# Performance work log

Measured on AMD Instinct MI355X. Metric: run time of the kernel, lower is better.

The kernel has to match this reference:

```python
import jax, jax.numpy as jnp
import numpy as np

VOCAB, HID, LSTM_H, T_LEN, N_LAB, BATCH = 21128, 768, 128, 256, 9, 32


def _gru_dir(x, Wih, Whh, bih, bhh):
    # x: [B,T,D]; PyTorch GRU gate order: reset, update, new
    xp = jnp.einsum('btd,gd->tbg', x, Wih) + bih  # [T,B,3H]
    H = Whh.shape[1]
    def step(h, xt):
        gh = h @ Whh.T + bhh
        xr, xz, xn = jnp.split(xt, 3, axis=-1)
        hr, hz, hn = jnp.split(gh, 3, axis=-1)
        r = jax.nn.sigmoid(xr + hr)
        z = jax.nn.sigmoid(xz + hz)
        n = jnp.tanh(xn + r * hn)
        hnew = (1.0 - z) * n + z * h
        return hnew, hnew
    h0 = jnp.zeros((x.shape[0], H), x.dtype)
    _, hs = jax.lax.scan(step, h0, xp)
    return hs  # [T,B,H]


def _crf_llh(emissions, labels, trans, start, end):
    # emissions [B,T,L], labels [B,T]; full mask (all ones)
    e = jnp.transpose(emissions, (1, 0, 2))  # [T,B,L]
    emit_scores = jnp.take_along_axis(e, labels.T[:, :, None], axis=2)[:, :, 0]  # [T,B]
    trans_scores = trans[labels[:, :-1], labels[:, 1:]]  # [B,T-1]
    num = start[labels[:, 0]] + emit_scores.sum(0) + trans_scores.sum(1) + end[labels[:, -1]]
    def step(alpha, et):
        alpha = jax.nn.logsumexp(alpha[:, :, None] + trans[None] + et[:, None, :], axis=1)
        return alpha, None
    alpha0 = start + e[0]
    alpha, _ = jax.lax.scan(step, alpha0, e[1:])
    denom = jax.nn.logsumexp(alpha + end, axis=1)
    return num - denom  # [B]


def _viterbi(emissions, trans, start, end):
    e = jnp.transpose(emissions, (1, 0, 2))  # [T,B,L]
    def step(alpha, et):
        scores = alpha[:, :, None] + trans[None]  # [B,L_prev,L_cur]
        bp = jnp.argmax(scores, axis=1)
        alpha = jnp.max(scores, axis=1) + et
        return alpha, bp
    alpha0 = start + e[0]
    alpha, bps = jax.lax.scan(step, alpha0, e[1:])  # bps: [T-1,B,L]
    last = jnp.argmax(alpha + end, axis=1)  # [B]
    def back(y, bp):
        yprev = jnp.take_along_axis(bp, y[:, None], axis=1)[:, 0]
        return yprev, yprev
    _, path = jax.lax.scan(back, last, bps, reverse=True)  # [T-1,B]
    return jnp.concatenate([path, last[None]], axis=0).T  # [B,T]


def setup_inputs() -> dict:
    key = jax.random.key(0)
    ks = jax.random.split(key, 16)
    s = 0.02
    inp = {
        'input_ids': jax.random.randint(ks[0], (BATCH, T_LEN), 0, VOCAB),
        'attention_mask': jnp.ones((BATCH, T_LEN), jnp.int64 if jax.config.jax_enable_x64 else jnp.int32),
        'labels': jax.random.randint(ks[1], (BATCH, T_LEN), 0, N_LAB),
        'emb': jax.random.normal(ks[2], (VOCAB, HID), jnp.float32) * s,
        'Wih_f': jax.random.normal(ks[3], (3 * LSTM_H, HID), jnp.float32) * s,
        'Whh_f': jax.random.normal(ks[4], (3 * LSTM_H, LSTM_H), jnp.float32) * s,
        'bih_f': jnp.zeros((3 * LSTM_H,), jnp.float32),
        'bhh_f': jnp.zeros((3 * LSTM_H,), jnp.float32),
        'Wih_b': jax.random.normal(ks[5], (3 * LSTM_H, HID), jnp.float32) * s,
        'Whh_b': jax.random.normal(ks[6], (3 * LSTM_H, LSTM_H), jnp.float32) * s,
        'bih_b': jnp.zeros((3 * LSTM_H,), jnp.float32),
        'bhh_b': jnp.zeros((3 * LSTM_H,), jnp.float32),
        'Wlin': jax.random.normal(ks[7], (N_LAB, 2 * LSTM_H), jnp.float32) * s,
        'blin': jnp.zeros((N_LAB,), jnp.float32),
        'trans': jax.random.normal(ks[8], (N_LAB, N_LAB), jnp.float32) * 0.1,
        'start': jax.random.normal(ks[9], (N_LAB,), jnp.float32) * 0.1,
        'end': jax.random.normal(ks[10], (N_LAB,), jnp.float32) * 0.1,
    }
    return inp


def reference(input_ids, attention_mask, labels, emb, Wih_f, Whh_f, bih_f, bhh_f,
              Wih_b, Whh_b, bih_b, bhh_b, Wlin, blin, trans, start, end):
    x = emb[input_ids]  # [B,T,HID]
    hf = _gru_dir(x, Wih_f, Whh_f, bih_f, bhh_f)                 # [T,B,H]
    hb = _gru_dir(x[:, ::-1, :], Wih_b, Whh_b, bih_b, bhh_b)[::-1]  # [T,B,H]
    seq = jnp.concatenate([hf, hb], axis=-1).transpose(1, 0, 2)  # [B,T,2H]
    emissions = seq @ Wlin.T + blin                              # [B,T,L]
    decoded = _viterbi(emissions, trans, start, end)             # [B,T] int
    llh = _crf_llh(emissions, labels, trans, start, end)         # [B]
    loss = -jnp.mean(llh)
    return decoded, loss
```

## Files before the change

### kernel.cpp

```cpp
#include <hip/hip_runtime.h>
#include <math.h>

#define T_LEN 256
#define BATCH 32
#define HID   768
#define GH    384
#define LH    128
#define NLAB  9
#define M_TOT (T_LEN*BATCH)

typedef float v2f __attribute__((ext_vector_type(2)));
typedef _Float16 h8 __attribute__((ext_vector_type(8)));
typedef float f4 __attribute__((ext_vector_type(4)));

#define LO_SCALE 1024.f
#define LO_INV   (1.f/1024.f)

#define BC(x, i) __int_as_float(__builtin_amdgcn_ds_swizzle(__float_as_int(x), (i) << 5))

#define BAR_LGKM() do {                                   \
    asm volatile("s_waitcnt lgkmcnt(0)" ::: "memory");    \
    __builtin_amdgcn_s_barrier();                         \
    asm volatile("" ::: "memory");                        \
  } while (0)

__global__ __launch_bounds__(256, 2) void k_gemm_xp(
    const int* __restrict__ ids, const float* __restrict__ emb,
    const float* __restrict__ Wf, const float* __restrict__ Wb,
    const float* __restrict__ bihf, const float* __restrict__ bihb,
    float* __restrict__ xp)
{
  __shared__ __align__(16) _Float16 Ah[128*40];
  __shared__ __align__(16) _Float16 Al[128*40];
  __shared__ __align__(16) _Float16 Bh[128*40];
  __shared__ __align__(16) _Float16 Bl[128*40];

  const int tid  = threadIdx.x;
  const int lane = tid & 63, w = tid >> 6;
  const int m0 = blockIdx.y * 128, n0 = blockIdx.x * 128;

  const int srow = tid >> 1, sk = (tid & 1) * 16;
  const int gm = m0 + srow;
  const int tok = ids[(gm & 31) * T_LEN + (gm >> 5)];
  const float* aG = emb + (size_t)tok * HID + sk;
  const int gn = n0 + srow;
  const float* bG = (gn < GH ? Wf + (size_t)gn * HID
                             : Wb + (size_t)(gn - GH) * HID) + sk;

  const int fr = lane & 15, fq = lane >> 4;
  const int mrow = (w & 1) * 64;
  const int ncol = (w >> 1) * 64;

  f4 acc[4][4];
  f4 acc2[4][4];
#pragma unroll
  for (int i = 0; i < 4; ++i)
#pragma unroll
    for (int j = 0; j < 4; ++j) { acc[i][j] = f4{0,0,0,0}; acc2[i][j] = f4{0,0,0,0}; }

  const int sb = srow * 40 + sk;

  float4 ra[4], rb[4];
#pragma unroll
  for (int c = 0; c < 4; ++c) {
    ra[c] = *reinterpret_cast<const float4*>(aG + 4 * c);
    rb[c] = *reinterpret_cast<const float4*>(bG + 4 * c);
  }

  for (int kt = 0; kt < HID / 32; ++kt) {
    BAR_LGKM();
#pragma unroll
    for (int m = 0; m < 2; ++m) {
      const float4* src = m ? rb : ra;
      _Float16* dsth = m ? Bh : Ah;
      _Float16* dstl = m ? Bl : Al;
#pragma unroll
      for (int seg = 0; seg < 2; ++seg) {
        float xs[8] = {src[2*seg].x, src[2*seg].y, src[2*seg].z, src[2*seg].w,
                       src[2*seg+1].x, src[2*seg+1].y, src[2*seg+1].z, src[2*seg+1].w};
        h8 hi, lo;
#pragma unroll
        for (int c = 0; c < 8; ++c) {
          _Float16 h = (_Float16)xs[c];
          hi[c] = h;
          lo[c] = (_Float16)((xs[c] - (float)h) * LO_SCALE);
        }
        *reinterpret_cast<h8*>(&dsth[sb + seg * 8]) = hi;
        *reinterpret_cast<h8*>(&dstl[sb + seg * 8]) = lo;
      }
    }
    if (kt + 1 < HID / 32) {
      const float* pa = aG + (kt + 1) * 32;
      const float* pb = bG + (kt + 1) * 32;
#pragma unroll
      for (int c = 0; c < 4; ++c) {
        ra[c] = *reinterpret_cast<const float4*>(pa + 4 * c);
        rb[c] = *reinterpret_cast<const float4*>(pb + 4 * c);
      }
    }
    BAR_LGKM();

    h8 fbh[4], fbl[4];
#pragma unroll
    for (int j = 0; j < 4; ++j) {
      const int off = (ncol + j * 16 + fr) * 40 + fq * 8;
      fbh[j] = *reinterpret_cast<const h8*>(&Bh[off]);
      fbl[j] = *reinterpret_cast<const h8*>(&Bl[off]);
    }
#pragma unroll
    for (int i = 0; i < 4; ++i) {
      const int off = (mrow + i * 16 + fr) * 40 + fq * 8;
      h8 fah = *reinterpret_cast<const h8*>(&Ah[off]);
      h8 fal = *reinterpret_cast<const h8*>(&Al[off]);
#pragma unroll
      for (int j = 0; j < 4; ++j) {
        acc[i][j]  = __builtin_amdgcn_mfma_f32_16x16x32_f16(fah, fbh[j], acc[i][j],  0, 0, 0);
        acc2[i][j] = __builtin_amdgcn_mfma_f32_16x16x32_f16(fah, fbl[j], acc2[i][j], 0, 0, 0);
        acc2[i][j] = __builtin_amdgcn_mfma_f32_16x16x32_f16(fal, fbh[j], acc2[i][j], 0, 0, 0);
      }
    }
  }

  float bcol[4];
#pragma unroll
  for (int j = 0; j < 4; ++j) {
    const int c = n0 + ncol + j * 16 + fr;
    bcol[j] = (c < GH) ? bihf[c] : bihb[c - GH];
  }
#pragma unroll
  for (int i = 0; i < 4; ++i)
#pragma unroll
    for (int j = 0; j < 4; ++j) {
      const int col = n0 + ncol + j * 16 + fr;
#pragma unroll
      for (int r = 0; r < 4; ++r) {
        const int row = m0 + mrow + i * 16 + fq * 4 + r;
        xp[(size_t)row * HID + col] = acc[i][j][r] + acc2[i][j][r] * LO_INV + bcol[j];
      }
    }
}

__global__ __attribute__((amdgpu_flat_work_group_size(512, 512),
                          amdgpu_waves_per_eu(2, 2)))
void k_gru(
    const float* __restrict__ xp,
    const float* __restrict__ Whhf, const float* __restrict__ Whhb,
    const float* __restrict__ bhhf, const float* __restrict__ bhhb,
    float* __restrict__ hbuf, float* __restrict__ lossp)
{
  __shared__ __align__(1024) float hsp[2][256];
  const int tid = threadIdx.x;
  const int g   = tid >> 2;
  const int q   = tid & 3;
  const int bd  = blockIdx.x;
  const int dir = bd >> 5, b = bd & 31;
  const float* Whh = dir ? Whhb : Whhf;
  const float* bhh = dir ? bhhb : bhhf;

  if (bd == 0 && tid == 0) *lossp = 0.f;

  const float br = bhh[g], bz = bhh[g + LH], bn = bhh[g + 2*LH];
  const float* wg0 = Whh + (size_t)(0*LH + g) * LH + q * 32;
  const float* wg1 = Whh + (size_t)(1*LH + g) * LH + q * 32;
  const float* wg2 = Whh + (size_t)(2*LH + g) * LH + q * 32;

  const int t0 = dir ? (T_LEN - 1) : 0;
  const int dt = dir ? -1 : 1;
  const float* px = xp + (size_t)t0 * BATCH * HID + b * HID + dir * GH + g;
  float*       ph = hbuf + (size_t)t0 * BATCH * 256 + b * 256 + dir * LH + g;

  const long long xs = (long long)dt * BATCH * HID * 4;
  const long long hs = (long long)dt * BATCH * 256 * 4;
  const unsigned xslo = (unsigned)(xs & 0xffffffffll);
  const int      xshi = (int)(xs >> 32);
  const unsigned hslo = (unsigned)(hs & 0xffffffffll);
  const int      hshi = (int)(hs >> 32);
  const unsigned xlo = (unsigned)(uintptr_t)px, xhi = (unsigned)((uintptr_t)px >> 32);
  const unsigned hlo = (unsigned)(uintptr_t)ph, hhi = (unsigned)((uintptr_t)ph >> 32);
  const unsigned rd0 = (unsigned)(uintptr_t)(&hsp[0][36 * q]);
  const unsigned wr0 = (unsigned)(uintptr_t)(&hsp[1][36 * (g >> 5) + (g & 31)]);

  if (tid < LH) hsp[0][36 * (tid >> 5) + (tid & 31)] = 0.f;
  BAR_LGKM();

  int cnt = T_LEN;
  asm volatile(
    "global_load_dwordx4 v[128:131], %[wg0], off\n\t"
    "global_load_dwordx4 v[132:135], %[wg0], off offset:16\n\t"
    "global_load_dwordx4 v[136:139], %[wg0], off offset:32\n\t"
    "global_load_dwordx4 v[140:143], %[wg0], off offset:48\n\t"
    "global_load_dwordx4 v[144:147], %[wg0], off offset:64\n\t"
    "global_load_dwordx4 v[148:151], %[wg0], off offset:80\n\t"
    "global_load_dwordx4 v[152:155], %[wg0], off offset:96\n\t"
    "global_load_dwordx4 v[156:159], %[wg0], off offset:112\n\t"
    "global_load_dwordx4 v[160:163], %[wg1], off\n\t"
    "global_load_dwordx4 v[164:167], %[wg1], off offset:16\n\t"
    "global_load_dwordx4 v[168:171], %[wg1], off offset:32\n\t"
    "global_load_dwordx4 v[172:175], %[wg1], off offset:48\n\t"
    "global_load_dwordx4 v[176:179], %[wg1], off offset:64\n\t"
    "global_load_dwordx4 v[180:183], %[wg1], off offset:80\n\t"
    "global_load_dwordx4 v[184:187], %[wg1], off offset:96\n\t"
    "global_load_dwordx4 v[188:191], %[wg1], off offset:112\n\t"
    "global_load_dwordx4 v[192:195], %[wg2], off\n\t"
    "global_load_dwordx4 v[196:199], %[wg2], off offset:16\n\t"
    "global_load_dwordx4 v[200:203], %[wg2], off offset:32\n\t"
    "global_load_dwordx4 v[204:207], %[wg2], off offset:48\n\t"
    "global_load_dwordx4 v[208:211], %[wg2], off offset:64\n\t"
    "global_load_dwordx4 v[212:215], %[wg2], off offset:80\n\t"
    "global_load_dwordx4 v[216:219], %[wg2], off offset:96\n\t"
    "global_load_dwordx4 v[220:223], %[wg2], off offset:112\n\t"
    "v_mov_b32 v96, %[xlo]\n\t"
    "v_mov_b32 v97, %[xhi]\n\t"
    "v_mov_b32 v98, %[hlo]\n\t"
    "v_mov_b32 v99, %[hhi]\n\t"
    "v_mov_b32 v100, %[rd0]\n\t"
    "v_mov_b32 v101, %[wr0]\n\t"
    "global_load_dword v107, v[96:97], off\n\t"
    "global_load_dword v108, v[96:97], off offset:512\n\t"
    "global_load_dword v109, v[96:97], off offset:1024\n\t"
    "v_mov_b32 v110, 0\n\t"
    "s_waitcnt vmcnt(0)\n\t"
    "0:\n\t"
    "s_waitcnt vmcnt(1)\n\t"
    "v_mov_b32 v104, v107\n\t"
    "v_mov_b32 v105, v108\n\t"
    "v_mov_b32 v106, v109\n\t"
    "ds_read_b128 v[224:227], v100\n\t"
    "ds_read_b128 v[228:231], v100 offset:16\n\t"
    "ds_read_b128 v[232:235], v100 offset:32\n\t"
    "ds_read_b128 v[236:239], v100 offset:48\n\t"
    "ds_read_b128 v[240:243], v100 offset:64\n\t"
    "ds_read_b128 v[244:247], v100 offset:80\n\t"
    "ds_read_b128 v[248:251], v100 offset:96\n\t"
    "ds_read_b128 v[252:255], v100 offset:112\n\t"
    "s_cmp_lg_u32 %[cnt], 1\n\t"
    "s_cbranch_scc0 2f\n\t"
    "v_add_co_u32 v96, vcc, %[xslo], v96\n\t"
    "v_addc_co_u32 v97, vcc, %[xshi], v97, vcc\n\t"
    "global_load_dword v107, v[96:97], off\n\t"
    "global_load_dword v108, v[96:97], off offset:512\n\t"
    "global_load_dword v109, v[96:97], off offset:1024\n\t"
    "2:\n\t"
    "s_waitcnt lgkmcnt(0)\n\t"
    "v_pk_mul_f32 v[116:117], v[128:129], v[224:225]\n\t"
    "v_pk_mul_f32 v[118:119], v[130:131], v[226:227]\n\t"
    "v_pk_fma_f32 v[116:117], v[132:133], v[228:229], v[116:117]\n\t"
    "v_pk_fma_f32 v[118:119], v[134:135], v[230:231], v[118:119]\n\t"
    "v_pk_fma_f32 v[116:117], v[136:137], v[232:233], v[116:117]\n\t"
    "v_pk_fma_f32 v[118:119], v[138:139], v[234:235], v[118:119]\n\t"
    "v_pk_fma_f32 v[116:117], v[140:141], v[236:237], v[116:117]\n\t"
    "v_pk_fma_f32 v[118:119], v[142:143], v[238:239], v[118:119]\n\t"
    "v_pk_fma_f32 v[116:117], v[144:145], v[240:241], v[116:117]\n\t"
    "v_pk_fma_f32 v[118:119], v[146:147], v[242:243], v[118:119]\n\t"
    "v_pk_fma_f32 v[116:117], v[148:149], v[244:245], v[116:117]\n\t"
    "v_pk_fma_f32 v[118:119], v[150:151], v[246:247], v[118:119]\n\t"
    "v_pk_fma_f32 v[116:117], v[152:153], v[248:249], v[116:117]\n\t"
    "v_pk_fma_f32 v[118:119], v[154:155], v[250:251], v[118:119]\n\t"
    "v_pk_fma_f32 v[116:117], v[156:157], v[252:253], v[116:117]\n\t"
    "v_pk_fma_f32 v[118:119], v[158:159], v[254:255], v[118:119]\n\t"
    "v_pk_mul_f32 v[120:121], v[160:161], v[224:225]\n\t"
    "v_pk_mul_f32 v[122:123], v[162:163], v[226:227]\n\t"
    "v_pk_fma_f32 v[120:121], v[164:165], v[228:229], v[120:121]\n\t"
    "v_pk_fma_f32 v[122:123], v[166:167], v[230:231], v[122:123]\n\t"
    "v_pk_fma_f32 v[120:121], v[168:169], v[232:233], v[120:121]\n\t"
    "v_pk_fma_f32 v[122:123], v[170:171], v[234:235], v[122:123]\n\t"
    "v_pk_fma_f32 v[120:121], v[172:173], v[236:237], v[120:121]\n\t"
    "v_pk_fma_f32 v[122:123], v[174:175], v[238:239], v[122:123]\n\t"
    "v_pk_fma_f32 v[120:121], v[176:177], v[240:241], v[120:121]\n\t"
    "v_pk_fma_f32 v[122:123], v[178:179], v[242:243], v[122:123]\n\t"
    "v_pk_fma_f32 v[120:121], v[180:181], v[244:245], v[120:121]\n\t"
    "v_pk_fma_f32 v[122:123], v[182:183], v[246:247], v[122:123]\n\t"
    "v_pk_fma_f32 v[120:121], v[184:185], v[248:249], v[120:121]\n\t"
    "v_pk_fma_f32 v[122:123], v[186:187], v[250:251], v[122:123]\n\t"
    "v_pk_fma_f32 v[120:121], v[188:189], v[252:253], v[120:121]\n\t"
    "v_pk_fma_f32 v[122:123], v[190:191], v[254:255], v[122:123]\n\t"
    "v_pk_mul_f32 v[124:125], v[192:193], v[224:225]\n\t"
    "v_pk_mul_f32 v[126:127], v[194:195], v[226:227]\n\t"
    "v_pk_fma_f32 v[124:125], v[196:197], v[228:229], v[124:125]\n\t"
    "v_pk_fma_f32 v[126:127], v[198:199], v[230:231], v[126:127]\n\t"
    "v_pk_fma_f32 v[124:125], v[200:201], v[232:233], v[124:125]\n\t"
    "v_pk_fma_f32 v[126:127], v[202:203], v[234:235], v[126:127]\n\t"
    "v_pk_fma_f32 v[124:125], v[204:205], v[236:237], v[124:125]\n\t"
    "v_pk_fma_f32 v[126:127], v[206:207], v[238:239], v[126:127]\n\t"
    "v_pk_fma_f32 v[124:125], v[208:209], v[240:241], v[124:125]\n\t"
    "v_pk_fma_f32 v[126:127], v[210:211], v[242:243], v[126:127]\n\t"
    "v_pk_fma_f32 v[124:125], v[212:213], v[244:245], v[124:125]\n\t"
    "v_pk_fma_f32 v[126:127], v[214:215], v[246:247], v[126:127]\n\t"
    "v_pk_fma_f32 v[124:125], v[216:217], v[248:249], v[124:125]\n\t"
    "v_pk_fma_f32 v[126:127], v[218:219], v[250:251], v[126:127]\n\t"
    "v_pk_fma_f32 v[124:125], v[220:221], v[252:253], v[124:125]\n\t"
    "v_pk_fma_f32 v[126:127], v[222:223], v[254:255], v[126:127]\n\t"
    "v_add_f32 v116, v116, v117\n\t"
    "v_add_f32 v118, v118, v119\n\t"
    "v_add_f32 v116, v116, v118\n\t"
    "v_add_f32 v120, v120, v121\n\t"
    "v_add_f32 v122, v122, v123\n\t"
    "v_add_f32 v120, v120, v122\n\t"
    "v_add_f32 v124, v124, v125\n\t"
    "v_add_f32 v126, v126, v127\n\t"
    "v_add_f32 v124, v124, v126\n\t"
    "ds_swizzle_b32 v111, v116 offset:0x041F\n\t"
    "ds_swizzle_b32 v112, v120 offset:0x041F\n\t"
    "ds_swizzle_b32 v113, v124 offset:0x041F\n\t"
    "s_waitcnt lgkmcnt(0)\n\t"
    "v_add_f32 v116, v116, v111\n\t"
    "v_add_f32 v120, v120, v112\n\t"
    "v_add_f32 v124, v124, v113\n\t"
    "ds_swizzle_b32 v111, v116 offset:0x081F\n\t"
    "ds_swizzle_b32 v112, v120 offset:0x081F\n\t"
    "ds_swizzle_b32 v113, v124 offset:0x081F\n\t"
    "s_waitcnt lgkmcnt(0)\n\t"
    "v_add_f32 v116, v116, v111\n\t"
    "v_add_f32 v120, v120, v112\n\t"
    "v_add_f32 v124, v124, v113\n\t"
    "v_add_f32 v111, v104, v116\n\t"
    "v_add_f32 v112, v105, v120\n\t"
    "v_add_f32 v113, v124, %[bn]\n\t"
    "v_add_f32 v111, v111, %[br]\n\t"
    "v_add_f32 v112, v112, %[bz]\n\t"
    "v_mul_f32 v111, 0xbfb8aa3b, v111\n\t"
    "v_mul_f32 v112, 0xbfb8aa3b, v112\n\t"
    "v_exp_f32 v111, v111\n\t"
    "v_exp_f32 v112, v112\n\t"
    "s_nop 0\n\t"
    "v_add_f32 v111, 1.0, v111\n\t"
    "v_add_f32 v112, 1.0, v112\n\t"
    "v_rcp_f32 v111, v111\n\t"
    "v_rcp_f32 v112, v112\n\t"
    "s_nop 0\n\t"
    "v_fmac_f32 v106, v111, v113\n\t"
    "v_mul_f32 v113, 0x4038aa3b, v106\n\t"
    "v_exp_f32 v113, v113\n\t"
    "v_sub_f32 v115, 1.0, v112\n\t"
    "s_nop 0\n\t"
    "v_add_f32 v114, -1.0, v113\n\t"
    "v_add_f32 v113, 1.0, v113\n\t"
    "v_rcp_f32 v113, v113\n\t"
    "s_nop 1\n\t"
    "v_mul_f32 v114, v114, v113\n\t"
    "v_mul_f32 v115, v115, v114\n\t"
    "v_fmac_f32 v115, v112, v110\n\t"
    "v_mov_b32 v110, v115\n\t"
    "ds_write_b32 v101, v115\n\t"
    "global_store_dword v[98:99], v115, off\n\t"
    "v_add_co_u32 v98, vcc, %[hslo], v98\n\t"
    "v_addc_co_u32 v99, vcc, %[hshi], v99, vcc\n\t"
    "v_xor_b32 v100, 0x400, v100\n\t"
    "v_xor_b32 v101, 0x400, v101\n\t"
    "s_waitcnt lgkmcnt(0)\n\t"
    "s_barrier\n\t"
    "s_sub_u32 %[cnt], %[cnt], 1\n\t"
    "s_cmp_lg_u32 %[cnt], 0\n\t"
    "s_cbranch_scc1 0b\n\t"
    : [cnt]"+s"(cnt)
    : [wg0]"v"(wg0), [wg1]"v"(wg1), [wg2]"v"(wg2),
      [xlo]"v"(xlo), [xhi]"v"(xhi), [hlo]"v"(hlo), [hhi]"v"(hhi),
      [rd0]"v"(rd0), [wr0]"v"(wr0),
      [br]"v"(br), [bz]"v"(bz), [bn]"v"(bn),
      [xslo]"s"(xslo), [xshi]"v"(xshi), [hslo]"s"(hslo), [hshi]"v"(hshi)
    : "memory", "vcc", "scc",
      "v96","v97","v98","v99","v100","v101","v102","v103","v104","v105",
      "v106","v107","v108","v109","v110","v111","v112","v113","v114","v115",
      "v116","v117","v118","v119","v120","v121","v122","v123","v124","v125",
      "v126","v127","v128","v129","v130","v131","v132","v133","v134","v135",
      "v136","v137","v138","v139","v140","v141","v142","v143","v144","v145",
      "v146","v147","v148","v149","v150","v151","v152","v153","v154","v155",
      "v156","v157","v158","v159","v160","v161","v162","v163","v164","v165",
      "v166","v167","v168","v169","v170","v171","v172","v173","v174","v175",
      "v176","v177","v178","v179","v180","v181","v182","v183","v184","v185",
      "v186","v187","v188","v189","v190","v191","v192","v193","v194","v195",
      "v196","v197","v198","v199","v200","v201","v202","v203","v204","v205",
      "v206","v207","v208","v209","v210","v211","v212","v213","v214","v215",
      "v216","v217","v218","v219","v220","v221","v222","v223","v224","v225",
      "v226","v227","v228","v229","v230","v231","v232","v233","v234","v235",
      "v236","v237","v238","v239","v240","v241","v242","v243","v244","v245",
      "v246","v247","v248","v249","v250","v251","v252","v253","v254","v255");
}

__global__ __launch_bounds__(256, 1) void k_crf_fused(
    const float* __restrict__ hbuf, const float* __restrict__ Wlin,
    const float* __restrict__ blin, const int* __restrict__ labels,
    const float* __restrict__ trans, const float* __restrict__ start,
    const float* __restrict__ endv, float* __restrict__ dec_out,
    float* __restrict__ lossp)
{
  __shared__ float el[T_LEN * 10];
  __shared__ __align__(16) unsigned char bp8[(T_LEN - 1) * 16];
  const int b    = blockIdx.x;
  const int tid  = threadIdx.x;
  const int lane = tid & 63, w = tid >> 6;
  const int sub  = lane >> 4, l16 = lane & 15;

  float4 wreg[NLAB][4];
#pragma unroll
  for (int j = 0; j < NLAB; ++j)
#pragma unroll
    for (int c = 0; c < 4; ++c)
      wreg[j][c] = *reinterpret_cast<const float4*>(Wlin + j * 256 + l16 * 16 + c * 4);

  for (int k = 0; k < 16; ++k) {
    const int t = w * 64 + k * 4 + sub;
    const float* hp = hbuf + ((size_t)t * BATCH + b) * 256 + l16 * 16;
    const float4 h0 = *reinterpret_cast<const float4*>(hp);
    const float4 h1 = *reinterpret_cast<const float4*>(hp + 4);
    const float4 h2 = *reinterpret_cast<const float4*>(hp + 8);
    const float4 h3 = *reinterpret_cast<const float4*>(hp + 12);
    float acc[NLAB];
#pragma unroll
    for (int j = 0; j < NLAB; ++j) {
      const float4 w0 = wreg[j][0], w1 = wreg[j][1], w2 = wreg[j][2], w3 = wreg[j][3];
      float s0 = h0.x*w0.x + h0.y*w0.y + h0.z*w0.z + h0.w*w0.w;
      float s1 = h1.x*w1.x + h1.y*w1.y + h1.z*w1.z + h1.w*w1.w;
      float s2 = h2.x*w2.x + h2.y*w2.y + h2.z*w2.z + h2.w*w2.w;
      float s3 = h3.x*w3.x + h3.y*w3.y + h3.z*w3.z + h3.w*w3.w;
      acc[j] = (s0 + s1) + (s2 + s3);
    }
#pragma unroll
    for (int j = 0; j < NLAB; ++j) {
#pragma unroll
      for (int off = 1; off < 16; off <<= 1)
        acc[j] += __shfl_xor(acc[j], off);
    }
    if (l16 < NLAB) {
      float v = acc[0];
#pragma unroll
      for (int j = 1; j < NLAB; ++j) v = (l16 == j) ? acc[j] : v;
      el[t * 10 + l16] = v + blin[l16];
    }
  }
  __syncthreads();

  if (w == 0) {
    float tcol[NLAB];
#pragma unroll
    for (int i = 0; i < NLAB; ++i)
      tcol[i] = (lane < NLAB) ? trans[i * NLAB + lane] : 0.f;
    float alpha = (lane < NLAB) ? (start[lane] + el[lane]) : -3e38f;
    float et_next = (lane < NLAB) ? el[10 + lane] : 0.f;
    for (int s = 0; s < T_LEN - 1; ++s) {
      const float et = et_next;
      if (s < T_LEN - 2)
        et_next = (lane < NLAB) ? el[(s + 2) * 10 + lane] : 0.f;
      float v[NLAB];
      v[0] = BC(alpha, 0) + tcol[0];
      v[1] = BC(alpha, 1) + tcol[1];
      v[2] = BC(alpha, 2) + tcol[2];
      v[3] = BC(alpha, 3) + tcol[3];
      v[4] = BC(alpha, 4) + tcol[4];
      v[5] = BC(alpha, 5) + tcol[5];
      v[6] = BC(alpha, 6) + tcol[6];
      v[7] = BC(alpha, 7) + tcol[7];
      v[8] = BC(alpha, 8) + tcol[8];
      float v01 = (v[0] >= v[1]) ? v[0] : v[1];  int i01 = (v[0] >= v[1]) ? 0 : 1;
      float v23 = (v[2] >= v[3]) ? v[2] : v[3];  int i23 = (v[2] >= v[3]) ? 2 : 3;
      float v45 = (v[4] >= v[5]) ? v[4] : v[5];  int i45 = (v[4] >= v[5]) ? 4 : 5;
      float v67 = (v[6] >= v[7]) ? v[6] : v[7];  int i67 = (v[6] >= v[7]) ? 6 : 7;
      float va = (v01 >= v23) ? v01 : v23;       int ia = (v01 >= v23) ? i01 : i23;
      float vb = (v45 >= v67) ? v45 : v67;       int ib = (v45 >= v67) ? i45 : i67;
      float vc = (va >= vb) ? va : vb;           int ic = (va >= vb) ? ia : ib;
      float best = (vc >= v[8]) ? vc : v[8];     int bi = (vc >= v[8]) ? ic : 8;
      alpha = best + et;
      if (lane < NLAB) bp8[s * 16 + lane] = (unsigned char)bi;
    }
    float fin = alpha + ((lane < NLAB) ? endv[lane] : 0.f);
    float fv[NLAB];
    fv[0] = BC(fin, 0); fv[1] = BC(fin, 1); fv[2] = BC(fin, 2);
    fv[3] = BC(fin, 3); fv[4] = BC(fin, 4); fv[5] = BC(fin, 5);
    fv[6] = BC(fin, 6); fv[7] = BC(fin, 7); fv[8] = BC(fin, 8);
    float f01 = (fv[0] >= fv[1]) ? fv[0] : fv[1];  int j01 = (fv[0] >= fv[1]) ? 0 : 1;
    float f23 = (fv[2] >= fv[3]) ? fv[2] : fv[3];  int j23 = (fv[2] >= fv[3]) ? 2 : 3;
    float f45 = (fv[4] >= fv[5]) ? fv[4] : fv[5];  int j45 = (fv[4] >= fv[5]) ? 4 : 5;
    float f67 = (fv[6] >= fv[7]) ? fv[6] : fv[7];  int j67 = (fv[6] >= fv[7]) ? 6 : 7;
    float fa = (f01 >= f23) ? f01 : f23;           int ja = (f01 >= f23) ? j01 : j23;
    float fb = (f45 >= f67) ? f45 : f67;           int jb = (f45 >= f67) ? j45 : j67;
    float fc = (fa >= fb) ? fa : fb;               int jc = (fa >= fb) ? ja : jb;
    int last = (fc >= fv[8]) ? jc : 8;
    if (lane == 0) {
      int y = last;
      dec_out[b * T_LEN + (T_LEN - 1)] = (float)y;
      uint4 row = *reinterpret_cast<const uint4*>(&bp8[(T_LEN - 2) * 16]);
      for (int s = T_LEN - 2; s >= 0; --s) {
        uint4 nrow = row;
        if (s > 0) nrow = *reinterpret_cast<const uint4*>(&bp8[(s - 1) * 16]);
        unsigned wsel = (y < 4) ? row.x : ((y < 8) ? row.y : row.z);
        y = (int)((wsel >> ((y & 3) * 8)) & 0xffu);
        dec_out[b * T_LEN + s] = (float)y;
        row = nrow;
      }
    }
  } else if (w == 1) {
    float tcol[NLAB];
#pragma unroll
    for (int i = 0; i < NLAB; ++i)
      tcol[i] = (lane < NLAB) ? trans[i * NLAB + lane] : 0.f;
    float ca = (lane < NLAB) ? (start[lane] + el[lane]) : -3e38f;
    float et_next = (lane < NLAB) ? el[10 + lane] : 0.f;
    for (int s = 0; s < T_LEN - 1; ++s) {
      const float et = et_next;
      if (s < T_LEN - 2)
        et_next = (lane < NLAB) ? el[(s + 2) * 10 + lane] : 0.f;
      float c[NLAB];
      c[0] = BC(ca, 0) + tcol[0];
      c[1] = BC(ca, 1) + tcol[1];
      c[2] = BC(ca, 2) + tcol[2];
      c[3] = BC(ca, 3) + tcol[3];
      c[4] = BC(ca, 4) + tcol[4];
      c[5] = BC(ca, 5) + tcol[5];
      c[6] = BC(ca, 6) + tcol[6];
      c[7] = BC(ca, 7) + tcol[7];
      c[8] = BC(ca, 8) + tcol[8];
      float m01 = fmaxf(c[0], c[1]), m23 = fmaxf(c[2], c[3]);
      float m45 = fmaxf(c[4], c[5]), m67 = fmaxf(c[6], c[7]);
      float m = fmaxf(fmaxf(fmaxf(m01, m23), fmaxf(m45, m67)), c[8]);
      float p0 = __expf(c[0]-m) + __expf(c[1]-m), p1 = __expf(c[2]-m) + __expf(c[3]-m);
      float p2 = __expf(c[4]-m) + __expf(c[5]-m), p3 = __expf(c[6]-m) + __expf(c[7]-m);
      float p = ((p0 + p1) + (p2 + p3)) + __expf(c[8]-m);
      ca = m + __logf(p) + et;
    }
    float fv[NLAB];
    fv[0] = BC(ca, 0) + endv[0];
    fv[1] = BC(ca, 1) + endv[1];
    fv[2] = BC(ca, 2) + endv[2];
    fv[3] = BC(ca, 3) + endv[3];
    fv[4] = BC(ca, 4) + endv[4];
    fv[5] = BC(ca, 5) + endv[5];
    fv[6] = BC(ca, 6) + endv[6];
    fv[7] = BC(ca, 7) + endv[7];
    fv[8] = BC(ca, 8) + endv[8];
    float mx = -3e38f;
#pragma unroll
    for (int j = 0; j < NLAB; ++j) mx = fmaxf(mx, fv[j]);
    float ps = 0.f;
#pragma unroll
    for (int j = 0; j < NLAB; ++j) ps += __expf(fv[j] - mx);
    float denom = mx + __logf(ps);

    const int* lb = labels + b * T_LEN;
    float part = 0.f;
    for (int t4 = 0; t4 < 4; ++t4) {
      int t = lane * 4 + t4;
      int l = lb[t];
      part += el[t * 10 + l];
      if (t > 0) part += trans[lb[t - 1] * NLAB + l];
    }
#pragma unroll
    for (int off = 32; off > 0; off >>= 1) part += __shfl_xor(part, off);
    if (lane == 0) {
      float num = part + start[lb[0]] + endv[lb[T_LEN - 1]];
      float llh = num - denom;
      atomicAdd(lossp, -llh * (1.0f / BATCH));
    }
  }
}

extern "C" void kernel_launch(void* const* d_in, const int* in_sizes, int n_in,
                              void* d_out, int out_size, void* d_ws, size_t ws_size,
                              hipStream_t stream) {
  const int*   ids    = (const int*)d_in[0];
  const int*   labels = (const int*)d_in[2];
  const float* emb    = (const float*)d_in[3];
  const float* Wihf   = (const float*)d_in[4];
  const float* Whhf   = (const float*)d_in[5];
  const float* bihf   = (const float*)d_in[6];
  const float* bhhf   = (const float*)d_in[7];
  const float* Wihb   = (const float*)d_in[8];
  const float* Whhb   = (const float*)d_in[9];
  const float* bihb   = (const float*)d_in[10];
  const float* bhhb   = (const float*)d_in[11];
  const float* Wlin   = (const float*)d_in[12];
  const float* blin   = (const float*)d_in[13];
  const float* trans  = (const float*)d_in[14];
  const float* start  = (const float*)d_in[15];
  const float* endv   = (const float*)d_in[16];

  float* xp    = (float*)d_ws;
  float* hbuf  = xp + (size_t)M_TOT * HID;
  float* out   = (float*)d_out;
  float* lossp = out + M_TOT;

  k_gemm_xp<<<dim3(6, 64), 256, 0, stream>>>(ids, emb, Wihf, Wihb, bihf, bihb, xp);
  k_gru<<<64, 512, 0, stream>>>(xp, Whhf, Whhb, bhhf, bhhb, hbuf, lossp);
  k_crf_fused<<<BATCH, 256, 0, stream>>>(hbuf, Wlin, blin, labels, trans,
                                         start, endv, out, lossp);
}
```

Before: 393.9 us.

## Use fp16 recurrent weights and hidden state with dot2 in GRU loop

Converts the recurrent Whh weights held in registers to packed fp16 and keeps the shared hidden state in fp16. The per-step matvec then uses v_dot2_f32_f16 with fp32 accumulation, halving the LDS read volume and the dependent FMA chain. It also frees registers, drops the padded LDS layout and removes the last-step load skip. The cost is fp16 rounding of weights and hidden state, which compounds over 256 recurrent steps and may move results away from the fp32 reference.

Measured after the change: 384.4 us. -2.4%, faster.

```diff
diff --git a/kernel.cpp b/kernel.cpp
--- a/kernel.cpp
+++ b/kernel.cpp
@@ -148,7 +148,7 @@
     const float* __restrict__ bhhf, const float* __restrict__ bhhb,
     float* __restrict__ hbuf, float* __restrict__ lossp)
 {
-  __shared__ __align__(1024) float hsp[2][256];
+  __shared__ __align__(1024) _Float16 hsp[2][256];
   const int tid = threadIdx.x;
   const int g   = tid >> 2;
   const int q   = tid & 3;
@@ -177,10 +177,10 @@
   const int      hshi = (int)(hs >> 32);
   const unsigned xlo = (unsigned)(uintptr_t)px, xhi = (unsigned)((uintptr_t)px >> 32);
   const unsigned hlo = (unsigned)(uintptr_t)ph, hhi = (unsigned)((uintptr_t)ph >> 32);
-  const unsigned rd0 = (unsigned)(uintptr_t)(&hsp[0][36 * q]);
-  const unsigned wr0 = (unsigned)(uintptr_t)(&hsp[1][36 * (g >> 5) + (g & 31)]);
-
-  if (tid < LH) hsp[0][36 * (tid >> 5) + (tid & 31)] = 0.f;
+  const unsigned rd0 = (unsigned)(uintptr_t)(&hsp[0][q * 32]);
+  const unsigned wr0 = (unsigned)(uintptr_t)(&hsp[1][g]);
+
+  if (tid < 128) reinterpret_cast<unsigned*>(&hsp[0][0])[tid] = 0u;
   BAR_LGKM();
 
   int cnt = T_LEN;
@@ -218,6 +218,55 @@
     "global_load_dword v107, v[96:97], off\n\t"
     "global_load_dword v108, v[96:97], off offset:512\n\t"
     "global_load_dword v109, v[96:97], off offset:1024\n\t"
+    "s_waitcnt vmcnt(3)\n\t"
+    "v_cvt_pkrtz_f16_f32 v128, v128, v129\n\t"
+    "v_cvt_pkrtz_f16_f32 v129, v130, v131\n\t"
+    "v_cvt_pkrtz_f16_f32 v130, v132, v133\n\t"
+    "v_cvt_pkrtz_f16_f32 v131, v134, v135\n\t"
+    "v_cvt_pkrtz_f16_f32 v132, v136, v137\n\t"
+    "v_cvt_pkrtz_f16_f32 v133, v138, v139\n\t"
+    "v_cvt_pkrtz_f16_f32 v134, v140, v141\n\t"
+    "v_cvt_pkrtz_f16_f32 v135, v142, v143\n\t"
+    "v_cvt_pkrtz_f16_f32 v136, v144, v145\n\t"
+    "v_cvt_pkrtz_f16_f32 v137, v146, v147\n\t"
+    "v_cvt_pkrtz_f16_f32 v138, v148, v149\n\t"
+    "v_cvt_pkrtz_f16_f32 v139, v150, v151\n\t"
+    "v_cvt_pkrtz_f16_f32 v140, v152, v153\n\t"
+    "v_cvt_pkrtz_f16_f32 v141, v154, v155\n\t"
+    "v_cvt_pkrtz_f16_f32 v142, v156, v157\n\t"
+    "v_cvt_pkrtz_f16_f32 v143, v158, v159\n\t"
+    "v_cvt_pkrtz_f16_f32 v144, v160, v161\n\t"
+    "v_cvt_pkrtz_f16_f32 v145, v162, v163\n\t"
+    "v_cvt_pkrtz_f16_f32 v146, v164, v165\n\t"
+    "v_cvt_pkrtz_f16_f32 v147, v166, v167\n\t"
+    "v_cvt_pkrtz_f16_f32 v148, v168, v169\n\t"
+    "v_cvt_pkrtz_f16_f32 v149, v170, v171\n\t"
+    "v_cvt_pkrtz_f16_f32 v150, v172, v173\n\t"
+    "v_cvt_pkrtz_f16_f32 v151, v174, v175\n\t"
+    "v_cvt_pkrtz_f16_f32 v152, v176, v177\n\t"
+    "v_cvt_pkrtz_f16_f32 v153, v178, v179\n\t"
+    "v_cvt_pkrtz_f16_f32 v154, v180, v181\n\t"
+    "v_cvt_pkrtz_f16_f32 v155, v182, v183\n\t"
+    "v_cvt_pkrtz_f16_f32 v156, v184, v185\n\t"
+    "v_cvt_pkrtz_f16_f32 v157, v186, v187\n\t"
+    "v_cvt_pkrtz_f16_f32 v158, v188, v189\n\t"
+    "v_cvt_pkrtz_f16_f32 v159, v190, v191\n\t"
+    "v_cvt_pkrtz_f16_f32 v160, v192, v193\n\t"
+    "v_cvt_pkrtz_f16_f32 v161, v194, v195\n\t"
+    "v_cvt_pkrtz_f16_f32 v162, v196, v197\n\t"
+    "v_cvt_pkrtz_f16_f32 v163, v198, v199\n\t"
+    "v_cvt_pkrtz_f16_f32 v164, v200, v201\n\t"
+    "v_cvt_pkrtz_f16_f32 v165, v202, v203\n\t"
+    "v_cvt_pkrtz_f16_f32 v166, v204, v205\n\t"
+    "v_cvt_pkrtz_f16_f32 v167, v206, v207\n\t"
+    "v_cvt_pkrtz_f16_f32 v168, v208, v209\n\t"
+    "v_cvt_pkrtz_f16_f32 v169, v210, v211\n\t"
+    "v_cvt_pkrtz_f16_f32 v170, v212, v213\n\t"
+    "v_cvt_pkrtz_f16_f32 v171, v214, v215\n\t"
+    "v_cvt_pkrtz_f16_f32 v172, v216, v217\n\t"
+    "v_cvt_pkrtz_f16_f32 v173, v218, v219\n\t"
+    "v_cvt_pkrtz_f16_f32 v174, v220, v221\n\t"
+    "v_cvt_pkrtz_f16_f32 v175, v222, v223\n\t"
     "v_mov_b32 v110, 0\n\t"
     "s_waitcnt vmcnt(0)\n\t"
     "0:\n\t"
@@ -225,97 +274,93 @@
     "v_mov_b32 v104, v107\n\t"
     "v_mov_b32 v105, v108\n\t"
     "v_mov_b32 v106, v109\n\t"
-    "ds_read_b128 v[224:227], v100\n\t"
-    "ds_read_b128 v[228:231], v100 offset:16\n\t"
-    "ds_read_b128 v[232:235], v100 offset:32\n\t"
-    "ds_read_b128 v[236:239], v100 offset:48\n\t"
-    "ds_read_b128 v[240:243], v100 offset:64\n\t"
-    "ds_read_b128 v[244:247], v100 offset:80\n\t"
-    "ds_read_b128 v[248:251], v100 offset:96\n\t"
-    "ds_read_b128 v[252:255], v100 offset:112\n\t"
-    "s_cmp_lg_u32 %[cnt], 1\n\t"
-    "s_cbranch_scc0 2f\n\t"
+    "ds_read_b128 v[176:179], v100\n\t"
+    "ds_read_b128 v[180:183], v100 offset:16\n\t"
+    "ds_read_b128 v[184:187], v100 offset:32\n\t"
+    "ds_read_b128 v[188:191], v100 offset:48\n\t"
+    "s_cmp_gt_u32 %[cnt], 1\n\t"
+    "s_cbranch_scc0 3f\n\t"
     "v_add_co_u32 v96, vcc, %[xslo], v96\n\t"
     "v_addc_co_u32 v97, vcc, %[xshi], v97, vcc\n\t"
+    "3:\n\t"
     "global_load_dword v107, v[96:97], off\n\t"
     "global_load_dword v108, v[96:97], off offset:512\n\t"
     "global_load_dword v109, v[96:97], off offset:1024\n\t"
-    "2:\n\t"
     "s_waitcnt lgkmcnt(0)\n\t"
-    "v_pk_mul_f32 v[116:117], v[128:129], v[224:225]\n\t"
-    "v_pk_mul_f32 v[118:119], v[130:131], v[226:227]\n\t"
-    "v_pk_fma_f32 v[116:117], v[132:133], v[228:229], v[116:117]\n\t"
-    "v_pk_fma_f32 v[118:119], v[134:135], v[230:231], v[118:119]\n\t"
-    "v_pk_fma_f32 v[116:117], v[136:137], v[232:233], v[116:117]\n\t"
-    "v_pk_fma_f32 v[118:119], v[138:139], v[234:235], v[118:119]\n\t"
-    "v_pk_fma_f32 v[116:117], v[140:141], v[236:237], v[116:117]\n\t"
-    "v_pk_fma_f32 v[118:119], v[142:143], v[238:239], v[118:119]\n\t"
-    "v_pk_fma_f32 v[116:117], v[144:145], v[240:241], v[116:117]\n\t"
-    "v_pk_fma_f32 v[118:119], v[146:147], v[242:243], v[118:119]\n\t"
-    "v_pk_fma_f32 v[116:117], v[148:149], v[244:245], v[116:117]\n\t"
-    "v_pk_fma_f32 v[118:119], v[150:151], v[246:247], v[118:119]\n\t"
-    "v_pk_fma_f32 v[116:117], v[152:153], v[248:249], v[116:117]\n\t"
-    "v_pk_fma_f32 v[118:119], v[154:155], v[250:251], v[118:119]\n\t"
-    "v_pk_fma_f32 v[116:117], v[156:157], v[252:253], v[116:117]\n\t"
-    "v_pk_fma_f32 v[118:119], v[158:159], v[254:255], v[118:119]\n\t"
-    "v_pk_mul_f32 v[120:121], v[160:161], v[224:225]\n\t"
-    "v_pk_mul_f32 v[122:123], v[162:163], v[226:227]\n\t"
-    "v_pk_fma_f32 v[120:121], v[164:165], v[228:229], v[120:121]\n\t"
-    "v_pk_fma_f32 v[122:123], v[166:167], v[230:231], v[122:123]\n\t"
-    "v_pk_fma_f32 v[120:121], v[168:169], v[232:233], v[120:121]\n\t"
-    "v_pk_fma_f32 v[122:123], v[170:171], v[234:235], v[122:123]\n\t"
-    "v_pk_fma_f32 v[120:121], v[172:173], v[236:237], v[120:121]\n\t"
-    "v_pk_fma_f32 v[122:123], v[174:175], v[238:239], v[122:123]\n\t"
-    "v_pk_fma_f32 v[120:121], v[176:177], v[240:241], v[120:121]\n\t"
-    "v_pk_fma_f32 v[122:123], v[178:179], v[242:243], v[122:123]\n\t"
-    "v_pk_fma_f32 v[120:121], v[180:181], v[244:245], v[120:121]\n\t"
-    "v_pk_fma_f32 v[122:123], v[182:183], v[246:247], v[122:123]\n\t"
-    "v_pk_fma_f32 v[120:121], v[184:185], v[248:249], v[120:121]\n\t"
-    "v_pk_fma_f32 v[122:123], v[186:187], v[250:251], v[122:123]\n\t"
-    "v_pk_fma_f32 v[120:121], v[188:189], v[252:253], v[120:121]\n\t"
-    "v_pk_fma_f32 v[122:123], v[190:191], v[254:255], v[122:123]\n\t"
-    "v_pk_mul_f32 v[124:125], v[192:193], v[224:225]\n\t"
-    "v_pk_mul_f32 v[126:127], v[194:195], v[226:227]\n\t"
-    "v_pk_fma_f32 v[124:125], v[196:197], v[228:229], v[124:125]\n\t"
-    "v_pk_fma_f32 v[126:127], v[198:199], v[230:231], v[126:127]\n\t"
-    "v_pk_fma_f32 v[124:125], v[200:201], v[232:233], v[124:125]\n\t"
-    "v_pk_fma_f32 v[126:127], v[202:203], v[234:235], v[126:127]\n\t"
-    "v_pk_fma_f32 v[124:125], v[204:205], v[236:237], v[124:125]\n\t"
-    "v_pk_fma_f32 v[126:127], v[206:207], v[238:239], v[126:127]\n\t"
-    "v_pk_fma_f32 v[124:125], v[208:209], v[240:241], v[124:125]\n\t"
-    "v_pk_fma_f32 v[126:127], v[210:211], v[242:243], v[126:127]\n\t"
-    "v_pk_fma_f32 v[124:125], v[212:213], v[244:245], v[124:125]\n\t"
-    "v_pk_fma_f32 v[126:127], v[214:215], v[246:247], v[126:127]\n\t"
-    "v_pk_fma_f32 v[124:125], v[216:217], v[248:249], v[124:125]\n\t"
-    "v_pk_fma_f32 v[126:127], v[218:219], v[250:251], v[126:127]\n\t"
-    "v_pk_fma_f32 v[124:125], v[220:221], v[252:253], v[124:125]\n\t"
-    "v_pk_fma_f32 v[126:127], v[222:223], v[254:255], v[126:127]\n\t"
+    "v_mov_b32 v116, 0\n\t"
+    "v_mov_b32 v117, 0\n\t"
+    "v_mov_b32 v118, 0\n\t"
+    "v_mov_b32 v119, 0\n\t"
+    "v_mov_b32 v120, 0\n\t"
+    "v_mov_b32 v121, 0\n\t"
+    "v_dot2_f32_f16 v116, v128, v176, v116\n\t"
+    "v_dot2_f32_f16 v118, v144, v176, v118\n\t"
+    "v_dot2_f32_f16 v120, v160, v176, v120\n\t"
+    "v_dot2_f32_f16 v117, v129, v177, v117\n\t"
+    "v_dot2_f32_f16 v119, v145, v177, v119\n\t"
+    "v_dot2_f32_f16 v121, v161, v177, v121\n\t"
+    "v_dot2_f32_f16 v116, v130, v178, v116\n\t"
+    "v_dot2_f32_f16 v118, v146, v178, v118\n\t"
+    "v_dot2_f32_f16 v120, v162, v178, v120\n\t"
+    "v_dot2_f32_f16 v117, v131, v179, v117\n\t"
+    "v_dot2_f32_f16 v119, v147, v179, v119\n\t"
+    "v_dot2_f32_f16 v121, v163, v179, v121\n\t"
+    "v_dot2_f32_f16 v116, v132, v180, v116\n\t"
+    "v_dot2_f32_f16 v118, v148, v180, v118\n\t"
+    "v_dot2_f32_f16 v120, v164, v180, v120\n\t"
+    "v_dot2_f32_f16 v117, v133, v181, v117\n\t"
+    "v_dot2_f32_f16 v119, v149, v181, v119\n\t"
+    "v_dot2_f32_f16 v121, v165, v181, v121\n\t"
+    "v_dot2_f32_f16 v116, v134, v182, v116\n\t"
+    "v_dot2_f32_f16 v118, v150, v182, v118\n\t"
+    "v_dot2_f32_f16 v120, v166, v182, v120\n\t"
+    "v_dot2_f32_f16 v117, v135, v183, v117\n\t"
+    "v_dot2_f32_f16 v119, v151, v183, v119\n\t"
+    "v_dot2_f32_f16 v121, v167, v183, v121\n\t"
+    "v_dot2_f32_f16 v116, v136, v184, v116\n\t"
+    "v_dot2_f32_f16 v118, v152, v184, v118\n\t"
+    "v_dot2_f32_f16 v120, v168, v184, v120\n\t"
+    "v_dot2_f32_f16 v117, v137, v185, v117\n\t"
+    "v_dot2_f32_f16 v119, v153, v185, v119\n\t"
+    "v_dot2_f32_f16 v121, v169, v185, v121\n\t"
+    "v_dot2_f32_f16 v116, v138, v186, v116\n\t"
+    "v_dot2_f32_f16 v118, v154, v186, v118\n\t"
+    "v_dot2_f32_f16 v120, v170, v186, v120\n\t"
+    "v_dot2_f32_f16 v117, v139, v187, v117\n\t"
+    "v_dot2_f32_f16 v119, v155, v187, v119\n\t"
+    "v_dot2_f32_f16 v121, v171, v187, v121\n\t"
+    "v_dot2_f32_f16 v116, v140, v188, v116\n\t"
+    "v_dot2_f32_f16 v118, v156, v188, v118\n\t"
+    "v_dot2_f32_f16 v120, v172, v188, v120\n\t"
+    "v_dot2_f32_f16 v117, v141, v189, v117\n\t"
+    "v_dot2_f32_f16 v119, v157, v189, v119\n\t"
+    "v_dot2_f32_f16 v121, v173, v189, v121\n\t"
+    "v_dot2_f32_f16 v116, v142, v190, v116\n\t"
+    "v_dot2_f32_f16 v118, v158, v190, v118\n\t"
+    "v_dot2_f32_f16 v120, v174, v190, v120\n\t"
+    "v_dot2_f32_f16 v117, v143, v191, v117\n\t"
+    "v_dot2_f32_f16 v119, v159, v191, v119\n\t"
+    "v_dot2_f32_f16 v121, v175, v191, v121\n\t"
     "v_add_f32 v116, v116, v117\n\t"
     "v_add_f32 v118, v118, v119\n\t"
-    "v_add_f32 v116, v116, v118\n\t"
     "v_add_f32 v120, v120, v121\n\t"
-    "v_add_f32 v122, v122, v123\n\t"
-    "v_add_f32 v120, v120, v122\n\t"
-    "v_add_f32 v124, v124, v125\n\t"
-    "v_add_f32 v126, v126, v127\n\t"
-    "v_add_f32 v124, v124, v126\n\t"
     "ds_swizzle_b32 v111, v116 offset:0x041F\n\t"
-    "ds_swizzle_b32 v112, v120 offset:0x041F\n\t"
-    "ds_swizzle_b32 v113, v124 offset:0x041F\n\t"
+    "ds_swizzle_b32 v112, v118 offset:0x041F\n\t"
+    "ds_swizzle_b32 v113, v120 offset:0x041F\n\t"
     "s_waitcnt lgkmcnt(0)\n\t"
     "v_add_f32 v116, v116, v111\n\t"
-    "v_add_f32 v120, v120, v112\n\t"
-    "v_add_f32 v124, v124, v113\n\t"
+    "v_add_f32 v118, v118, v112\n\t"
+    "v_add_f32 v120, v120, v113\n\t"
     "ds_swizzle_b32 v111, v116 offset:0x081F\n\t"
-    "ds_swizzle_b32 v112, v120 offset:0x081F\n\t"
-    "ds_swizzle_b32 v113, v124 offset:0x081F\n\t"
+    "ds_swizzle_b32 v112, v118 offset:0x081F\n\t"
+    "ds_swizzle_b32 v113, v120 offset:0x081F\n\t"
     "s_waitcnt lgkmcnt(0)\n\t"
     "v_add_f32 v116, v116, v111\n\t"
-    "v_add_f32 v120, v120, v112\n\t"
-    "v_add_f32 v124, v124, v113\n\t"
+    "v_add_f32 v118, v118, v112\n\t"
+    "v_add_f32 v120, v120, v113\n\t"
     "v_add_f32 v111, v104, v116\n\t"
-    "v_add_f32 v112, v105, v120\n\t"
-    "v_add_f32 v113, v124, %[bn]\n\t"
+    "v_add_f32 v112, v105, v118\n\t"
+    "v_add_f32 v113, v120, %[bn]\n\t"
     "v_add_f32 v111, v111, %[br]\n\t"
     "v_add_f32 v112, v112, %[bz]\n\t"
     "v_mul_f32 v111, 0xbfb8aa3b, v111\n\t"
@@ -341,12 +386,13 @@
     "v_mul_f32 v115, v115, v114\n\t"
     "v_fmac_f32 v115, v112, v110\n\t"
     "v_mov_b32 v110, v115\n\t"
-    "ds_write_b32 v101, v115\n\t"
+    "v_cvt_f16_f32 v114, v115\n\t"
     "global_store_dword v[98:99], v115, off\n\t"
     "v_add_co_u32 v98, vcc, %[hslo], v98\n\t"
     "v_addc_co_u32 v99, vcc, %[hshi], v99, vcc\n\t"
-    "v_xor_b32 v100, 0x400, v100\n\t"
-    "v_xor_b32 v101, 0x400, v101\n\t"
+    "ds_write_b16 v101, v114\n\t"
+    "v_xor_b32 v100, 0x200, v100\n\t"
+    "v_xor_b32 v101, 0x200, v101\n\t"
     "s_waitcnt lgkmcnt(0)\n\t"
     "s_barrier\n\t"
     "s_sub_u32 %[cnt], %[cnt], 1\n\t"
@@ -371,10 +417,7 @@
       "v186","v187","v188","v189","v190","v191","v192","v193","v194","v195",
       "v196","v197","v198","v199","v200","v201","v202","v203","v204","v205",
       "v206","v207","v208","v209","v210","v211","v212","v213","v214","v215",
-      "v216","v217","v218","v219","v220","v221","v222","v223","v224","v225",
-      "v226","v227","v228","v229","v230","v231","v232","v233","v234","v235",
-      "v236","v237","v238","v239","v240","v241","v242","v243","v244","v245",
-      "v246","v247","v248","v249","v250","v251","v252","v253","v254","v255");
+      "v216","v217","v218","v219","v220","v221","v222","v223");
 }
 
 __global__ __launch_bounds__(256, 1) void k_crf_fused(
```
